# Performance work log

Measured on AMD Instinct MI355X. Metric: run time of the kernel, lower is better.

Reference implementation:

```python
import jax, jax.numpy as jnp
import numpy as np

N_CLASS = 32000
EMB = 1024
HID = 1024
BATCH = 256
SEQ = 256


def setup_inputs() -> dict:
    key = jax.random.key(0)
    ks = jax.random.split(key, 16)
    s = 0.02
    inp = {
        "X": jax.random.randint(ks[0], (BATCH, SEQ), 0, N_CLASS, dtype=jnp.int32),
        "C": jax.random.normal(ks[1], (N_CLASS, EMB), dtype=jnp.float32) * s,
    }
    gate_names = ["W_i1", "W_f1", "W_o1", "W_g1", "W_i2", "W_f2", "W_o2", "W_g2"]
    for i, n in enumerate(gate_names):
        inp[n] = jax.random.normal(ks[2 + i], (HID, EMB + HID), dtype=jnp.float32) * s
    # biases are initialized to ones in the original module
    for n in ["b_i1", "b_f1", "b_o1", "b_g1", "b_i2", "b_f2", "b_o2", "b_g2"]:
        inp[n] = jnp.ones((HID,), dtype=jnp.float32)
    inp["W_out"] = jax.random.normal(ks[10], (N_CLASS, HID), dtype=jnp.float32) * s
    inp["b_out"] = jnp.ones((N_CLASS,), dtype=jnp.float32)
    return inp


def _lstm_dir(Xt, Wi, bi, Wf, bf, Wo, bo, Wg, bg):
    """Run one LSTM direction over Xt: [T, B, E]. Returns final hidden [B, H]."""
    B = Xt.shape[1]
    H = bi.shape[0]
    h0 = jnp.zeros((B, H), Xt.dtype)
    c0 = jnp.zeros((B, H), Xt.dtype)

    def step(carry, x):
        h, c = carry
        xh = jnp.concatenate([x, h], axis=1)  # [B, E+H]
        i = jax.nn.sigmoid(xh @ Wi.T + bi)
        f = jax.nn.sigmoid(xh @ Wf.T + bf)
        o = jax.nn.sigmoid(xh @ Wo.T + bo)
        g = jnp.tanh(xh @ Wg.T + bg)
        c_new = f * c + i * g
        h_new = o * jnp.tanh(c_new)
        return (h_new, c_new), None

    (h, c), _ = jax.lax.scan(step, (h0, c0), Xt)
    return h


def reference(X, C, W_i1, W_f1, W_o1, W_g1, W_i2, W_f2, W_o2, W_g2,
              b_i1, b_f1, b_o1, b_g1, b_i2, b_f2, b_o2, b_g2, W_out, b_out):
    E = C[X]                       # [B, S, E] embedding lookup
    Xt = jnp.transpose(E, (1, 0, 2))  # [T, B, E]
    # forward direction
    h1 = _lstm_dir(Xt, W_i1, b_i1, W_f1, b_f1, W_o1, b_o1, W_g1, b_g1)
    # backward direction: original code detaches (numpy round-trip) before reversing
    Xr = jax.lax.stop_gradient(Xt)[::-1]
    h2 = _lstm_dir(Xr, W_i2, b_i2, W_f2, b_f2, W_o2, b_o2, W_g2, b_g2)
    return (h1 + h2) @ W_out.T + b_out  # [B, n_class]
```

## Files before the change

kernel.cpp:

```cpp
#include <hip/hip_runtime.h>
#include <hip/hip_bf16.h>
#include <stdint.h>
#include <math.h>

#define BATCH 256
#define SEQ   256
#define EMB   1024
#define HID   1024
#define NCLASS 32000
#define KTOT  2048
#define NGATE 8192

typedef __attribute__((ext_vector_type(8))) short bf16x8;
typedef __attribute__((ext_vector_type(4))) float f32x4;

__device__ __forceinline__ unsigned short f2b(float f) {
  union { float f; unsigned u; } v; v.f = f;
  unsigned r = v.u + 0x7FFFu + ((v.u >> 16) & 1u);
  return (unsigned short)(r >> 16);
}
__device__ __forceinline__ float b2f(unsigned short s) {
  union { unsigned u; float f; } v; v.u = ((unsigned)s) << 16;
  return v.f;
}
__device__ __forceinline__ void load_lds16(const void* g, void* l) {
  __builtin_amdgcn_global_load_lds(
      (const __attribute__((address_space(1))) unsigned int*)g,
      (__attribute__((address_space(3))) unsigned int*)l, 16, 0, 0);
}

__global__ void embed_kernel(const int* __restrict__ X, const float* __restrict__ C,
                             unsigned short* __restrict__ Xt) {
  int n = blockIdx.x;
  int t = n >> 8, b = n & 255;
  int tok = X[(size_t)b * SEQ + t];
  float4 v = ((const float4*)(C + (size_t)tok * EMB))[threadIdx.x];
  ushort4 o;
  o.x = f2b(v.x); o.y = f2b(v.y); o.z = f2b(v.z); o.w = f2b(v.w);
  ((ushort4*)(Xt + (size_t)n * EMB))[threadIdx.x] = o;
}

__global__ void castf_kernel(const float* __restrict__ src, unsigned short* __restrict__ dst,
                             int n4) {
  int i = blockIdx.x * blockDim.x + threadIdx.x;
  if (i < n4) {
    float4 v = ((const float4*)src)[i];
    ushort4 o;
    o.x = f2b(v.x); o.y = f2b(v.y); o.z = f2b(v.z); o.w = f2b(v.w);
    ((ushort4*)dst)[i] = o;
  }
}

__global__ void bcat_kernel(const float* b0, const float* b1, const float* b2,
                            const float* b3, const float* b4, const float* b5,
                            const float* b6, const float* b7, float* __restrict__ bcat) {
  int n = blockIdx.x * 256 + threadIdx.x;
  const float* bp[8] = {b0, b1, b2, b3, b4, b5, b6, b7};
  bcat[n] = bp[n >> 10][n & 1023];
}

__launch_bounds__(256)
__global__ void gx_gemm_kernel(const unsigned short* __restrict__ A,
                               const unsigned short* __restrict__ Bw,
                               const float* __restrict__ bcat,
                               unsigned short* __restrict__ Gx) {
  __shared__ unsigned short As[2][128][64];
  __shared__ unsigned short Bs[2][128][64];
  int bid = blockIdx.x;
  int m0 = (bid >> 6) * 128;
  int n0 = (bid & 63) * 128;
  int tid = threadIdx.x;

  auto stage = [&](int buf, int kb) {
    int kbase = kb * 64;
#pragma unroll
    for (int ri = 0; ri < 4; ++ri) {
      int slot = ri * 256 + tid;
      int row = slot >> 3;
      int ce  = (slot & 7) * 8;
      load_lds16(A + (size_t)(m0 + row) * EMB + kbase + ce, &As[buf][row][ce]);
    }
#pragma unroll
    for (int ri = 0; ri < 4; ++ri) {
      int slot = ri * 256 + tid;
      int row = slot >> 3;
      int ce  = (slot & 7) * 8;
      load_lds16(Bw + (size_t)(n0 + row) * KTOT + kbase + ce, &Bs[buf][row][ce]);
    }
  };

  int w = tid >> 6, lane = tid & 63;
  int lm = lane & 15, lq = lane >> 4;
  int wm = w & 1, wn = w >> 1;

  f32x4 zero = {0.f, 0.f, 0.f, 0.f};
  f32x4 acc[4][4];
#pragma unroll
  for (int mi = 0; mi < 4; ++mi)
#pragma unroll
    for (int ni = 0; ni < 4; ++ni) acc[mi][ni] = zero;

  stage(0, 0);
  for (int kb = 0; kb < 16; ++kb) {
    int cur = kb & 1;
    __syncthreads();
    if (kb + 1 < 16) stage(1 - cur, kb + 1);
#pragma unroll
    for (int kc = 0; kc < 2; ++kc) {
      bf16x8 af[4];
#pragma unroll
      for (int mi = 0; mi < 4; ++mi)
        af[mi] = *(const bf16x8*)&As[cur][wm * 64 + mi * 16 + lm][kc * 32 + lq * 8];
#pragma unroll
      for (int ni = 0; ni < 4; ++ni) {
        bf16x8 bb = *(const bf16x8*)&Bs[cur][wn * 64 + ni * 16 + lm][kc * 32 + lq * 8];
#pragma unroll
        for (int mi = 0; mi < 4; ++mi)
          acc[mi][ni] = __builtin_amdgcn_mfma_f32_16x16x32_bf16(af[mi], bb, acc[mi][ni], 0, 0, 0);
      }
    }
  }

#pragma unroll
  for (int ni = 0; ni < 4; ++ni) {
    int n = n0 + wn * 64 + ni * 16 + lm;
    float bn = bcat[n];
#pragma unroll
    for (int mi = 0; mi < 4; ++mi) {
#pragma unroll
      for (int reg = 0; reg < 4; ++reg) {
        int m = m0 + wm * 64 + mi * 16 + lq * 4 + reg;
        Gx[(size_t)m * NGATE + n] = f2b(acc[mi][ni][reg] + bn);
      }
    }
  }
}

#define BM 128
#define BN 64
#define BK 64
__launch_bounds__(256)
__global__ void lstm_step_kernel(const unsigned short* __restrict__ Xt,
                                 const unsigned short* __restrict__ Wcat,
                                 const unsigned short* __restrict__ Gx,
                                 const unsigned short* __restrict__ h_in,
                                 unsigned short* __restrict__ h_out,
                                 float* __restrict__ c_st,
                                 const float* __restrict__ b0, const float* __restrict__ b1,
                                 const float* __restrict__ b2, const float* __restrict__ b3,
                                 const float* __restrict__ b4, const float* __restrict__ b5,
                                 const float* __restrict__ b6, const float* __restrict__ b7,
                                 int t) {
  __shared__ unsigned short As[2][BM][BK];
  __shared__ unsigned short Bs[2][BN][BK];

  int bid = blockIdx.x;
  int d   = bid >> 7;
  int r   = bid & 127;
  int m0  = (r & 1) * BM;
  int j0  = (r >> 1) * 16;
  int td  = d ? (SEQ - 1 - t) : t;
  int tid = threadIdx.x;

  bool useGx = (Gx != nullptr);
  int  kiters = useGx ? (HID / BK) : (KTOT / BK);
  int  koff   = useGx ? EMB : 0;

  const unsigned short* Asrc0 = Xt  + ((size_t)td * BATCH + m0) * EMB;
  const unsigned short* Asrc1 = h_in + ((size_t)d * BATCH + m0) * HID;
  const unsigned short* Wd    = Wcat + (size_t)d * 4 * HID * KTOT;

  auto stageA = [&](int buf, int kb) {
    int kbase = kb * BK;
    const unsigned short* src; int ko;
    if (useGx)            { src = Asrc1; ko = kbase; }
    else if (kbase < EMB) { src = Asrc0; ko = kbase; }
    else                  { src = Asrc1; ko = kbase - EMB; }
#pragma unroll
    for (int ri = 0; ri < 4; ++ri) {
      int slot = ri * 256 + tid;
      int row = slot >> 3;
      int ce  = (slot & 7) * 8;
      load_lds16(src + (size_t)row * 1024 + ko + ce, &As[buf][row][ce]);
    }
  };
  auto stageB = [&](int buf, int kb) {
    int kbase = koff + kb * BK;
#pragma unroll
    for (int ri = 0; ri < 2; ++ri) {
      int slot = ri * 256 + tid;
      int rr  = slot >> 3;
      int g8  = rr >> 4;
      int jj  = rr & 15;
      int ce  = (slot & 7) * 8;
      load_lds16(Wd + (size_t)(g8 * HID + j0 + jj) * KTOT + kbase + ce, &Bs[buf][rr][ce]);
    }
  };

  int w = tid >> 6, lane = tid & 63;
  int lm = lane & 15, lq = lane >> 4;

  f32x4 zero = {0.f, 0.f, 0.f, 0.f};
  f32x4 acc[2][4];
#pragma unroll
  for (int mi = 0; mi < 2; ++mi)
#pragma unroll
    for (int g8 = 0; g8 < 4; ++g8) acc[mi][g8] = zero;

  stageA(0, 0); stageB(0, 0);
  for (int kb = 0; kb < kiters; ++kb) {
    int cur = kb & 1;
    __syncthreads();
    if (kb + 1 < kiters) { stageA(1 - cur, kb + 1); stageB(1 - cur, kb + 1); }
#pragma unroll
    for (int kc = 0; kc < 2; ++kc) {
      bf16x8 a0 = *(const bf16x8*)&As[cur][w * 32 +  0 + lm][kc * 32 + lq * 8];
      bf16x8 a1 = *(const bf16x8*)&As[cur][w * 32 + 16 + lm][kc * 32 + lq * 8];
#pragma unroll
      for (int g8 = 0; g8 < 4; ++g8) {
        bf16x8 bb = *(const bf16x8*)&Bs[cur][g8 * 16 + lm][kc * 32 + lq * 8];
        acc[0][g8] = __builtin_amdgcn_mfma_f32_16x16x32_bf16(a0, bb, acc[0][g8], 0, 0, 0);
        acc[1][g8] = __builtin_amdgcn_mfma_f32_16x16x32_bf16(a1, bb, acc[1][g8], 0, 0, 0);
      }
    }
  }

  const float* bi = d ? b4 : b0;
  const float* bf = d ? b5 : b1;
  const float* bo = d ? b6 : b2;
  const float* bgp= d ? b7 : b3;
  int j = j0 + lm;
  float vbi, vbf, vbo, vbg;
  if (!useGx) { vbi = bi[j]; vbf = bf[j]; vbo = bo[j]; vbg = bgp[j]; }
  else        { vbi = vbf = vbo = vbg = 0.f; }
  const unsigned short* gxb = nullptr;
  if (useGx)
    gxb = Gx + (size_t)td * BATCH * NGATE + (size_t)d * 4096 + j0 + lm;

#pragma unroll
  for (int mi = 0; mi < 2; ++mi) {
#pragma unroll
    for (int reg = 0; reg < 4; ++reg) {
      int b = m0 + w * 32 + mi * 16 + lq * 4 + reg;
      float pi = acc[mi][0][reg] + vbi;
      float pf = acc[mi][1][reg] + vbf;
      float po = acc[mi][2][reg] + vbo;
      float pg = acc[mi][3][reg] + vbg;
      if (useGx) {
        const unsigned short* g = gxb + (size_t)b * NGATE;
        pi += b2f(g[0]);
        pf += b2f(g[1024]);
        po += b2f(g[2048]);
        pg += b2f(g[3072]);
      }
      float ig = 1.f / (1.f + __expf(-pi));
      float fg = 1.f / (1.f + __expf(-pf));
      float og = 1.f / (1.f + __expf(-po));
      float gg = tanhf(pg);
      size_t ci = ((size_t)d * BATCH + b) * HID + j;
      float cn = fg * c_st[ci] + ig * gg;
      c_st[ci] = cn;
      h_out[ci] = f2b(og * tanhf(cn));
    }
  }
}

__global__ void hsum_kernel(const unsigned short* __restrict__ hfin,
                            unsigned short* __restrict__ hs) {
  int i = blockIdx.x * 256 + threadIdx.x;
  ushort4 a = ((const ushort4*)hfin)[i];
  ushort4 b = ((const ushort4*)(hfin + (size_t)BATCH * HID))[i];
  ushort4 o;
  o.x = f2b(b2f(a.x) + b2f(b.x));
  o.y = f2b(b2f(a.y) + b2f(b.y));
  o.z = f2b(b2f(a.z) + b2f(b.z));
  o.w = f2b(b2f(a.w) + b2f(b.w));
  ((ushort4*)hs)[i] = o;
}

__launch_bounds__(256)
__global__ void out_gemm_kernel(const unsigned short* __restrict__ A,
                                const unsigned short* __restrict__ B,
                                const float* __restrict__ bias,
                                float* __restrict__ Cout) {
  __shared__ unsigned short As[2][128][64];
  __shared__ unsigned short Bs[2][128][64];
  int bid = blockIdx.x;
  int m0 = (bid & 1) * 128;
  int n0 = (bid >> 1) * 128;
  int tid = threadIdx.x;

  auto stage = [&](int buf, int kb) {
    int kbase = kb * 64;
#pragma unroll
    for (int ri = 0; ri < 4; ++ri) {
      int slot = ri * 256 + tid;
      int row = slot >> 3;
      int ce  = (slot & 7) * 8;
      load_lds16(A + ((size_t)(m0 + row)) * HID + kbase + ce, &As[buf][row][ce]);
    }
#pragma unroll
    for (int ri = 0; ri < 4; ++ri) {
      int slot = ri * 256 + tid;
      int row = slot >> 3;
      int ce  = (slot & 7) * 8;
      load_lds16(B + ((size_t)(n0 + row)) * HID + kbase + ce, &Bs[buf][row][ce]);
    }
  };

  int w = tid >> 6, lane = tid & 63;
  int lm = lane & 15, lq = lane >> 4;
  int wm = w & 1, wn = w >> 1;

  f32x4 zero = {0.f, 0.f, 0.f, 0.f};
  f32x4 acc[4][4];
#pragma unroll
  for (int mi = 0; mi < 4; ++mi)
#pragma unroll
    for (int ni = 0; ni < 4; ++ni) acc[mi][ni] = zero;

  stage(0, 0);
  for (int kb = 0; kb < 16; ++kb) {
    int cur = kb & 1;
    __syncthreads();
    if (kb + 1 < 16) stage(1 - cur, kb + 1);
#pragma unroll
    for (int kc = 0; kc < 2; ++kc) {
      bf16x8 af[4];
#pragma unroll
      for (int mi = 0; mi < 4; ++mi)
        af[mi] = *(const bf16x8*)&As[cur][wm * 64 + mi * 16 + lm][kc * 32 + lq * 8];
#pragma unroll
      for (int ni = 0; ni < 4; ++ni) {
        bf16x8 bb = *(const bf16x8*)&Bs[cur][wn * 64 + ni * 16 + lm][kc * 32 + lq * 8];
#pragma unroll
        for (int mi = 0; mi < 4; ++mi)
          acc[mi][ni] = __builtin_amdgcn_mfma_f32_16x16x32_bf16(af[mi], bb, acc[mi][ni], 0, 0, 0);
      }
    }
  }

#pragma unroll
  for (int ni = 0; ni < 4; ++ni) {
    int n = n0 + wn * 64 + ni * 16 + lm;
    float bn = bias[n];
#pragma unroll
    for (int mi = 0; mi < 4; ++mi) {
#pragma unroll
      for (int reg = 0; reg < 4; ++reg) {
        int m = m0 + wm * 64 + mi * 16 + lq * 4 + reg;
        Cout[(size_t)m * NCLASS + n] = acc[mi][ni][reg] + bn;
      }
    }
  }
}

extern "C" void kernel_launch(void* const* d_in, const int* in_sizes, int n_in,
                              void* d_out, int out_size, void* d_ws, size_t ws_size,
                              hipStream_t stream) {
  const int*   X    = (const int*)d_in[0];
  const float* C    = (const float*)d_in[1];
  const float* Wg[8];
  for (int i = 0; i < 8; ++i) Wg[i] = (const float*)d_in[2 + i];
  const float* bg[8];
  for (int i = 0; i < 8; ++i) bg[i] = (const float*)d_in[10 + i];
  const float* Wout = (const float*)d_in[18];
  const float* bout = (const float*)d_in[19];
  float* out = (float*)d_out;

  const size_t szXt   = (size_t)SEQ * BATCH * EMB * 2;
  const size_t szWcat = (size_t)8 * HID * KTOT * 2;
  const size_t szWob  = (size_t)NCLASS * HID * 2;
  const size_t szH    = (size_t)2 * BATCH * HID * 2;
  const size_t szC    = (size_t)2 * BATCH * HID * 4;
  const size_t szHs   = (size_t)BATCH * HID * 2;
  const size_t szBc   = (size_t)NGATE * 4;
  const size_t szGx   = (size_t)SEQ * BATCH * NGATE * 2;

  uint8_t* p = (uint8_t*)d_ws;
  unsigned short* Xt   = (unsigned short*)p; p += szXt;
  unsigned short* Wcat = (unsigned short*)p; p += szWcat;
  unsigned short* Wob  = (unsigned short*)p; p += szWob;
  unsigned short* hb0  = (unsigned short*)p; p += szH;
  unsigned short* hb1  = (unsigned short*)p; p += szH;
  float*          cst  = (float*)p;          p += szC;
  unsigned short* hs   = (unsigned short*)p; p += szHs;
  float*          bcat = (float*)p;          p += szBc;
  unsigned short* Gx   = (unsigned short*)p; p += szGx;

  size_t need_full = (size_t)(p - (uint8_t*)d_ws);
  bool useGx = (ws_size >= need_full);
  if (!useGx) Gx = nullptr;

  hipMemsetAsync(hb0, 0, szH, stream);
  hipMemsetAsync(cst, 0, szC, stream);

  embed_kernel<<<SEQ * BATCH, 256, 0, stream>>>(X, C, Xt);
  for (int i = 0; i < 8; ++i)
    castf_kernel<<<2048, 256, 0, stream>>>(Wg[i], Wcat + (size_t)i * HID * KTOT,
                                           (HID * KTOT) / 4);
  castf_kernel<<<32000, 256, 0, stream>>>(Wout, Wob, (NCLASS * HID) / 4);

  if (useGx) {
    bcat_kernel<<<NGATE / 256, 256, 0, stream>>>(bg[0], bg[1], bg[2], bg[3],
                                                 bg[4], bg[5], bg[6], bg[7], bcat);
    gx_gemm_kernel<<<512 * 64, 256, 0, stream>>>(Xt, Wcat, bcat, Gx);
  }

  unsigned short* hbuf[2] = {hb0, hb1};
  for (int t = 0; t < SEQ; ++t) {
    lstm_step_kernel<<<256, 256, 0, stream>>>(
        Xt, Wcat, Gx, hbuf[t & 1], hbuf[(t + 1) & 1], cst,
        bg[0], bg[1], bg[2], bg[3], bg[4], bg[5], bg[6], bg[7], t);
  }
  hsum_kernel<<<256, 256, 0, stream>>>(hb0, hs);
  out_gemm_kernel<<<500, 256, 0, stream>>>(hs, Wob, bout, out);
}
```

Before: 10.52 ms.

## Replace per-step LSTM launches with persistent kernel holding recurrent weights in LDS

Replaces the 256 per-timestep kernel launches with a single persistent kernel of 256 blocks. Each block keeps its slice of the recurrent weights resident in LDS (128KB) and keeps the cell state in registers. Blocks synchronise between timesteps with a per-group global atomic barrier. The input-projection GEMM output is re-laid out so each block reads its gate values contiguously. This removes launch overhead and the repeated reloading of recurrent weights from global memory. In exchange it relies on all blocks being co-resident, and it uses fast tanh approximations.

```diff
diff --git a/kernel.cpp b/kernel.cpp
--- a/kernel.cpp
+++ b/kernel.cpp
@@ -27,6 +27,9 @@
   __builtin_amdgcn_global_load_lds(
       (const __attribute__((address_space(1))) unsigned int*)g,
       (__attribute__((address_space(3))) unsigned int*)l, 16, 0, 0);
+}
+__device__ __forceinline__ float tanh_fast(float x) {
+  return 1.f - 2.f / (__expf(2.f * x) + 1.f);
 }
 
 __global__ void embed_kernel(const int* __restrict__ X, const float* __restrict__ C,
@@ -63,7 +66,7 @@
 __global__ void gx_gemm_kernel(const unsigned short* __restrict__ A,
                                const unsigned short* __restrict__ Bw,
                                const float* __restrict__ bcat,
-                               unsigned short* __restrict__ Gx) {
+                               unsigned short* __restrict__ Gx2) {
   __shared__ unsigned short As[2][128][64];
   __shared__ unsigned short Bs[2][128][64];
   int bid = blockIdx.x;
@@ -121,18 +124,171 @@
     }
   }
 
+  int tt  = m0 >> 8;
+  int mhb = m0 & 255;
 #pragma unroll
   for (int ni = 0; ni < 4; ++ni) {
-    int n = n0 + wn * 64 + ni * 16 + lm;
+    int n  = n0 + wn * 64 + ni * 16 + lm;
     float bn = bcat[n];
+    int nb  = n0 + wn * 64 + ni * 16;
+    int d   = nb >> 12;
+    int g   = (nb >> 10) & 3;
+    int ugx = (nb >> 4) & 63;
+    unsigned short* gdst = Gx2 +
+        (((size_t)(tt * 2 + d) * 64 + ugx) * 256) * 64 + g * 16 + lm;
 #pragma unroll
     for (int mi = 0; mi < 4; ++mi) {
 #pragma unroll
       for (int reg = 0; reg < 4; ++reg) {
-        int m = m0 + wm * 64 + mi * 16 + lq * 4 + reg;
-        Gx[(size_t)m * NGATE + n] = f2b(acc[mi][ni][reg] + bn);
-      }
-    }
+        int bloc = mhb + wm * 64 + mi * 16 + lq * 4 + reg;
+        gdst[(size_t)bloc * 64] = f2b(acc[mi][ni][reg] + bn);
+      }
+    }
+  }
+}
+
+__launch_bounds__(256, 1)
+__global__ void lstm_persist(const unsigned short* __restrict__ Wcat,
+                             const unsigned short* __restrict__ Gx2,
+                             unsigned short* __restrict__ hb0,
+                             unsigned short* __restrict__ hb1,
+                             unsigned int* __restrict__ bar) {
+  __shared__ unsigned short Wlds[64 * 1024];
+  __shared__ unsigned short As[2][4096];
+
+  const int bid = blockIdx.x;
+  const int dir = bid >> 7;
+  const int mh  = (bid >> 6) & 1;
+  const int ug  = bid & 63;
+  const int j0  = ug * 16;
+  const int grp = bid >> 6;
+  const int tid = threadIdx.x;
+  const int w   = tid >> 6;
+  const int lane = tid & 63;
+  const int lm = lane & 15, lq = lane >> 4;
+
+  const unsigned short* Wd = Wcat + (size_t)dir * 4 * HID * KTOT;
+
+#pragma unroll
+  for (int i = 0; i < 32; ++i) {
+    int s = i * 256 + tid;
+    int P = s << 4;
+    int n = P >> 11;
+    int offl = (P & 2047) ^ ((n & 7) << 4);
+    int g = n >> 4, u = n & 15;
+    load_lds16(Wd + (size_t)(g * HID + j0 + u) * KTOT + EMB + (offl >> 1),
+               Wlds + (P >> 1));
+  }
+
+  int sp0 = 0, sp1 = 0, lp0 = 0, lp1 = 0;
+#pragma unroll
+  for (int r = 0; r < 2; ++r) {
+    int s = r * 256 + tid;
+    int P = s << 4;
+    int r2 = (P >> 8) & 1;
+    int r1 = (P >> 7) & 1;
+    int r0 = ((P >> 6) & 1) ^ r2;
+    int L  = P ^ ((r0 | (r1 << 1) | (r2 << 2)) << 4);
+    int row  = L >> 6;
+    int colb = L & 63;
+    if (r == 0) { sp0 = row * HID + (colb >> 1); lp0 = P >> 1; }
+    else        { sp1 = row * HID + (colb >> 1); lp1 = P >> 1; }
+  }
+
+  int row0 = w * 32 + lm;
+  int row1 = row0 + 16;
+  int aP0 = ((row0 * 64 + lq * 16) ^ ((row0 & 7) << 4)) >> 1;
+  int aP1 = ((row1 * 64 + lq * 16) ^ ((row1 & 7) << 4)) >> 1;
+  int swzB = (lm & 7) << 4;
+
+  float cs[2][4];
+#pragma unroll
+  for (int mi = 0; mi < 2; ++mi)
+#pragma unroll
+    for (int reg = 0; reg < 4; ++reg) cs[mi][reg] = 0.f;
+
+  const int rbb = w * 32 + lq * 4;
+  const size_t hblk = ((size_t)dir * 256 + mh * 128) * 1024;
+  unsigned int tgt = 0;
+  unsigned int* barp = bar + grp * 32;
+
+  __syncthreads();
+
+  for (int t = 0; t < SEQ; ++t) {
+    int td = dir ? (SEQ - 1 - t) : t;
+    const unsigned short* hprev = ((t & 1) ? hb1 : hb0) + hblk;
+    unsigned short*       hnext = ((t & 1) ? hb0 : hb1) + hblk;
+
+    const unsigned short* gxt = Gx2 +
+        ((((size_t)td * 2 + dir) * 64 + ug) * 256 + mh * 128) * 64 + lm;
+    unsigned short gxr[2][4][4];
+#pragma unroll
+    for (int mi = 0; mi < 2; ++mi)
+#pragma unroll
+      for (int reg = 0; reg < 4; ++reg) {
+        const unsigned short* gp = gxt + (size_t)(rbb + mi * 16 + reg) * 64;
+#pragma unroll
+        for (int g = 0; g < 4; ++g) gxr[mi][g][reg] = gp[g * 16];
+      }
+
+    f32x4 acc[2][4];
+#pragma unroll
+    for (int mi = 0; mi < 2; ++mi)
+#pragma unroll
+      for (int g = 0; g < 4; ++g) acc[mi][g] = (f32x4){0.f, 0.f, 0.f, 0.f};
+
+    if (t) {
+      load_lds16(hprev + sp0, &As[0][0] + lp0);
+      load_lds16(hprev + sp1, &As[0][0] + lp1);
+      for (int kb = 0; kb < 32; ++kb) {
+        int cur = kb & 1;
+        __syncthreads();
+        if (kb + 1 < 32) {
+          const unsigned short* hsrc = hprev + (kb + 1) * 32;
+          load_lds16(hsrc + sp0, &As[1 - cur][0] + lp0);
+          load_lds16(hsrc + sp1, &As[1 - cur][0] + lp1);
+        }
+        bf16x8 a0 = *(const bf16x8*)&As[cur][aP0];
+        bf16x8 a1 = *(const bf16x8*)&As[cur][aP1];
+        int off = ((kb * 64 + lq * 16) ^ swzB) >> 1;
+#pragma unroll
+        for (int g = 0; g < 4; ++g) {
+          bf16x8 bb = *(const bf16x8*)&Wlds[(g * 16 + lm) * 1024 + off];
+          acc[0][g] = __builtin_amdgcn_mfma_f32_16x16x32_bf16(a0, bb, acc[0][g], 0, 0, 0);
+          acc[1][g] = __builtin_amdgcn_mfma_f32_16x16x32_bf16(a1, bb, acc[1][g], 0, 0, 0);
+        }
+      }
+    }
+
+#pragma unroll
+    for (int mi = 0; mi < 2; ++mi) {
+#pragma unroll
+      for (int reg = 0; reg < 4; ++reg) {
+        float pi = acc[mi][0][reg] + b2f(gxr[mi][0][reg]);
+        float pf = acc[mi][1][reg] + b2f(gxr[mi][1][reg]);
+        float po = acc[mi][2][reg] + b2f(gxr[mi][2][reg]);
+        float pg = acc[mi][3][reg] + b2f(gxr[mi][3][reg]);
+        float ig = 1.f / (1.f + __expf(-pi));
+        float fg = 1.f / (1.f + __expf(-pf));
+        float og = 1.f / (1.f + __expf(-po));
+        float gg = tanh_fast(pg);
+        float cn = fg * cs[mi][reg] + ig * gg;
+        cs[mi][reg] = cn;
+        int rb = rbb + mi * 16 + reg;
+        hnext[(size_t)rb * 1024 + j0 + lm] = f2b(og * tanh_fast(cn));
+      }
+    }
+
+    tgt += 64;
+    __syncthreads();
+    if (tid == 0) {
+      __threadfence();
+      atomicAdd(barp, 1u);
+      while (__hip_atomic_load(barp, __ATOMIC_RELAXED,
+                               __HIP_MEMORY_SCOPE_AGENT) < tgt) {}
+    }
+    __syncthreads();
+    __threadfence();
   }
 }
 
@@ -233,9 +389,6 @@
   float vbi, vbf, vbo, vbg;
   if (!useGx) { vbi = bi[j]; vbf = bf[j]; vbo = bo[j]; vbg = bgp[j]; }
   else        { vbi = vbf = vbo = vbg = 0.f; }
-  const unsigned short* gxb = nullptr;
-  if (useGx)
-    gxb = Gx + (size_t)td * BATCH * NGATE + (size_t)d * 4096 + j0 + lm;
 
 #pragma unroll
   for (int mi = 0; mi < 2; ++mi) {
@@ -246,13 +399,6 @@
       float pf = acc[mi][1][reg] + vbf;
       float po = acc[mi][2][reg] + vbo;
       float pg = acc[mi][3][reg] + vbg;
-      if (useGx) {
-        const unsigned short* g = gxb + (size_t)b * NGATE;
-        pi += b2f(g[0]);
-        pf += b2f(g[1024]);
-        po += b2f(g[2048]);
-        pg += b2f(g[3072]);
-      }
       float ig = 1.f / (1.f + __expf(-pi));
       float fg = 1.f / (1.f + __expf(-pf));
       float og = 1.f / (1.f + __expf(-po));
@@ -405,13 +551,15 @@
     bcat_kernel<<<NGATE / 256, 256, 0, stream>>>(bg[0], bg[1], bg[2], bg[3],
                                                  bg[4], bg[5], bg[6], bg[7], bcat);
     gx_gemm_kernel<<<512 * 64, 256, 0, stream>>>(Xt, Wcat, bcat, Gx);
-  }
-
-  unsigned short* hbuf[2] = {hb0, hb1};
-  for (int t = 0; t < SEQ; ++t) {
-    lstm_step_kernel<<<256, 256, 0, stream>>>(
-        Xt, Wcat, Gx, hbuf[t & 1], hbuf[(t + 1) & 1], cst,
-        bg[0], bg[1], bg[2], bg[3], bg[4], bg[5], bg[6], bg[7], t);
+    unsigned int* bar = (unsigned int*)cst;
+    lstm_persist<<<256, 256, 0, stream>>>(Wcat, Gx, hb0, hb1, bar);
+  } else {
+    unsigned short* hbuf[2] = {hb0, hb1};
+    for (int t = 0; t < SEQ; ++t) {
+      lstm_step_kernel<<<256, 256, 0, stream>>>(
+          Xt, Wcat, Gx, hbuf[t & 1], hbuf[(t + 1) & 1], cst,
+          bg[0], bg[1], bg[2], bg[3], bg[4], bg[5], bg[6], bg[7], t);
+    }
   }
   hsum_kernel<<<256, 256, 0, stream>>>(hb0, hs);
   out_gemm_kernel<<<500, 256, 0, stream>>>(hs, Wob, bout, out);
```

After: 10.41 ms. About the same (-1.1%).

## Replace per-step LSTM launches with persistent kernel holding Wh in LDS

Applied to the files above, without the earlier changes.

Replaces the precomputed Gx GEMM and the 256 per-timestep launches with one persistent kernel of 256 blocks. Each block keeps its slice of the recurrent weights resident in a swizzled 128KB LDS buffer and holds the cell state in registers. The next step's input projection is computed while waiting on per-group atomic flags, so it overlaps the cross-block sync. This removes the large Gx round trip through memory and the launch overhead. The risks are that all blocks must be co-resident for the spin barrier, the spin loop has a bounded iteration count, and tanh now uses a fast exp-based approximation.

```diff
diff --git a/kernel.cpp b/kernel.cpp
--- a/kernel.cpp
+++ b/kernel.cpp
@@ -9,7 +9,6 @@
 #define HID   1024
 #define NCLASS 32000
 #define KTOT  2048
-#define NGATE 8192
 
 typedef __attribute__((ext_vector_type(8))) short bf16x8;
 typedef __attribute__((ext_vector_type(4))) float f32x4;
@@ -27,6 +26,9 @@
   __builtin_amdgcn_global_load_lds(
       (const __attribute__((address_space(1))) unsigned int*)g,
       (__attribute__((address_space(3))) unsigned int*)l, 16, 0, 0);
+}
+__device__ __forceinline__ float tanh_fast(float x) {
+  return 1.f - 2.f / (__expf(2.f * x) + 1.f);
 }
 
 __global__ void embed_kernel(const int* __restrict__ X, const float* __restrict__ C,
@@ -51,216 +53,181 @@
   }
 }
 
-__global__ void bcat_kernel(const float* b0, const float* b1, const float* b2,
-                            const float* b3, const float* b4, const float* b5,
-                            const float* b6, const float* b7, float* __restrict__ bcat) {
-  int n = blockIdx.x * 256 + threadIdx.x;
-  const float* bp[8] = {b0, b1, b2, b3, b4, b5, b6, b7};
-  bcat[n] = bp[n >> 10][n & 1023];
-}
-
-__launch_bounds__(256)
-__global__ void gx_gemm_kernel(const unsigned short* __restrict__ A,
-                               const unsigned short* __restrict__ Bw,
-                               const float* __restrict__ bcat,
-                               unsigned short* __restrict__ Gx) {
-  __shared__ unsigned short As[2][128][64];
-  __shared__ unsigned short Bs[2][128][64];
-  int bid = blockIdx.x;
-  int m0 = (bid >> 6) * 128;
-  int n0 = (bid & 63) * 128;
-  int tid = threadIdx.x;
-
-  auto stage = [&](int buf, int kb) {
-    int kbase = kb * 64;
-#pragma unroll
-    for (int ri = 0; ri < 4; ++ri) {
-      int slot = ri * 256 + tid;
-      int row = slot >> 3;
-      int ce  = (slot & 7) * 8;
-      load_lds16(A + (size_t)(m0 + row) * EMB + kbase + ce, &As[buf][row][ce]);
-    }
-#pragma unroll
-    for (int ri = 0; ri < 4; ++ri) {
-      int slot = ri * 256 + tid;
-      int row = slot >> 3;
-      int ce  = (slot & 7) * 8;
-      load_lds16(Bw + (size_t)(n0 + row) * KTOT + kbase + ce, &Bs[buf][row][ce]);
+__launch_bounds__(256, 1)
+__global__ void lstm_persist2(const unsigned short* __restrict__ Xt,
+                              const unsigned short* __restrict__ Wcat,
+                              const float* __restrict__ b0, const float* __restrict__ b1,
+                              const float* __restrict__ b2, const float* __restrict__ b3,
+                              const float* __restrict__ b4, const float* __restrict__ b5,
+                              const float* __restrict__ b6, const float* __restrict__ b7,
+                              unsigned short* __restrict__ hb0,
+                              unsigned short* __restrict__ hb1,
+                              unsigned int* __restrict__ flags) {
+  __shared__ unsigned short Whlds[64 * 1024];
+  __shared__ unsigned short Bxs[2][4096];
+
+  const int bid = blockIdx.x;
+  const int dir = bid >> 7;
+  const int mh  = (bid >> 6) & 1;
+  const int ug  = bid & 63;
+  const int j0  = ug * 16;
+  const int tid = threadIdx.x;
+  const int w   = tid >> 6;
+  const int lane = tid & 63;
+  const int lm = lane & 15, lq = lane >> 4;
+
+  const unsigned short* Wd = Wcat + (size_t)dir * 4 * HID * KTOT;
+
+#pragma unroll
+  for (int i = 0; i < 32; ++i) {
+    int P = (i * 256 + tid) << 4;
+    int row = P >> 11;
+    int offl = (P & 2047) ^ ((row & 7) << 4);
+    int g = row >> 4, u = row & 15;
+    load_lds16(Wd + (size_t)(g * HID + j0 + u) * KTOT + EMB + (offl >> 1),
+               &Whlds[P >> 1]);
+  }
+
+  const unsigned short* bxsrc[2];
+  int bxdst[2];
+#pragma unroll
+  for (int r = 0; r < 2; ++r) {
+    int P = (r * 256 + tid) << 4;
+    int row = P >> 7;
+    int L = P ^ ((row & 7) << 4);
+    int g = row >> 4, u = row & 15;
+    bxsrc[r] = Wd + (size_t)(g * HID + j0 + u) * KTOT + ((L & 127) >> 1);
+    bxdst[r] = P >> 1;
+  }
+
+  const int swz = (lm & 7) << 4;
+  const int r0off = (w * 32 + lm) * 1024 + lq * 8;
+  const int r1off = r0off + 16 * 1024;
+
+  const float* pbi = dir ? b4 : b0;
+  const float* pbf = dir ? b5 : b1;
+  const float* pbo = dir ? b6 : b2;
+  const float* pbg = dir ? b7 : b3;
+  const float vbi = pbi[j0 + lm], vbf = pbf[j0 + lm];
+  const float vbo = pbo[j0 + lm], vbg = pbg[j0 + lm];
+
+  f32x4 acc[2][4];
+  float cs[2][4];
+#pragma unroll
+  for (int mi = 0; mi < 2; ++mi)
+#pragma unroll
+    for (int reg = 0; reg < 4; ++reg) cs[mi][reg] = 0.f;
+
+  const size_t hblk = ((size_t)dir * BATCH + mh * 128) * HID;
+  unsigned int* fgrp = flags + (bid & ~63);
+  const int rbb = w * 32 + lq * 4;
+
+  auto xphase = [&](int td) {
+    const unsigned short* xs = Xt + ((size_t)td * BATCH + mh * 128) * EMB;
+#pragma unroll
+    for (int mi = 0; mi < 2; ++mi)
+#pragma unroll
+      for (int g = 0; g < 4; ++g) acc[mi][g] = (f32x4){0.f, 0.f, 0.f, 0.f};
+    load_lds16(bxsrc[0], &Bxs[0][bxdst[0]]);
+    load_lds16(bxsrc[1], &Bxs[0][bxdst[1]]);
+    bf16x8 xc00 = *(const bf16x8*)(xs + r0off);
+    bf16x8 xc01 = *(const bf16x8*)(xs + r1off);
+    bf16x8 xc10 = *(const bf16x8*)(xs + r0off + 32);
+    bf16x8 xc11 = *(const bf16x8*)(xs + r1off + 32);
+#pragma unroll
+    for (int ch = 0; ch < 16; ++ch) {
+      int cur = ch & 1;
+      __syncthreads();
+      bf16x8 xn00 = xc00, xn01 = xc01, xn10 = xc10, xn11 = xc11;
+      if (ch < 15) {
+        load_lds16(bxsrc[0] + (ch + 1) * 64, &Bxs[1 - cur][bxdst[0]]);
+        load_lds16(bxsrc[1] + (ch + 1) * 64, &Bxs[1 - cur][bxdst[1]]);
+        int ko = (ch + 1) * 64;
+        xn00 = *(const bf16x8*)(xs + r0off + ko);
+        xn01 = *(const bf16x8*)(xs + r1off + ko);
+        xn10 = *(const bf16x8*)(xs + r0off + ko + 32);
+        xn11 = *(const bf16x8*)(xs + r1off + ko + 32);
+      }
+#pragma unroll
+      for (int kc = 0; kc < 2; ++kc) {
+        bf16x8 a0 = kc ? xc10 : xc00;
+        bf16x8 a1 = kc ? xc11 : xc01;
+#pragma unroll
+        for (int g = 0; g < 4; ++g) {
+          int offB = (((g * 16 + lm) * 128 + kc * 64 + lq * 16) ^ swz) >> 1;
+          bf16x8 bb = *(const bf16x8*)&Bxs[cur][offB];
+          acc[0][g] = __builtin_amdgcn_mfma_f32_16x16x32_bf16(a0, bb, acc[0][g], 0, 0, 0);
+          acc[1][g] = __builtin_amdgcn_mfma_f32_16x16x32_bf16(a1, bb, acc[1][g], 0, 0, 0);
+        }
+      }
+      xc00 = xn00; xc01 = xn01; xc10 = xn10; xc11 = xn11;
     }
   };
 
-  int w = tid >> 6, lane = tid & 63;
-  int lm = lane & 15, lq = lane >> 4;
-  int wm = w & 1, wn = w >> 1;
-
-  f32x4 zero = {0.f, 0.f, 0.f, 0.f};
-  f32x4 acc[4][4];
-#pragma unroll
-  for (int mi = 0; mi < 4; ++mi)
-#pragma unroll
-    for (int ni = 0; ni < 4; ++ni) acc[mi][ni] = zero;
-
-  stage(0, 0);
-  for (int kb = 0; kb < 16; ++kb) {
-    int cur = kb & 1;
-    __syncthreads();
-    if (kb + 1 < 16) stage(1 - cur, kb + 1);
-#pragma unroll
-    for (int kc = 0; kc < 2; ++kc) {
-      bf16x8 af[4];
-#pragma unroll
-      for (int mi = 0; mi < 4; ++mi)
-        af[mi] = *(const bf16x8*)&As[cur][wm * 64 + mi * 16 + lm][kc * 32 + lq * 8];
-#pragma unroll
-      for (int ni = 0; ni < 4; ++ni) {
-        bf16x8 bb = *(const bf16x8*)&Bs[cur][wn * 64 + ni * 16 + lm][kc * 32 + lq * 8];
-#pragma unroll
-        for (int mi = 0; mi < 4; ++mi)
-          acc[mi][ni] = __builtin_amdgcn_mfma_f32_16x16x32_bf16(af[mi], bb, acc[mi][ni], 0, 0, 0);
-      }
-    }
-  }
-
-#pragma unroll
-  for (int ni = 0; ni < 4; ++ni) {
-    int n = n0 + wn * 64 + ni * 16 + lm;
-    float bn = bcat[n];
-#pragma unroll
-    for (int mi = 0; mi < 4; ++mi) {
+  auto hphase = [&](const unsigned short* hp) {
+    bf16x8 ac0 = *(const bf16x8*)(hp + r0off);
+    bf16x8 ac1 = *(const bf16x8*)(hp + r1off);
+#pragma unroll
+    for (int kb = 0; kb < 32; ++kb) {
+      bf16x8 an0 = ac0, an1 = ac1;
+      if (kb < 31) {
+        an0 = *(const bf16x8*)(hp + r0off + (kb + 1) * 32);
+        an1 = *(const bf16x8*)(hp + r1off + (kb + 1) * 32);
+      }
+      int offW = ((kb * 64 + lq * 16) ^ swz) >> 1;
+#pragma unroll
+      for (int g = 0; g < 4; ++g) {
+        bf16x8 bb = *(const bf16x8*)&Whlds[(g * 16 + lm) * 1024 + offW];
+        acc[0][g] = __builtin_amdgcn_mfma_f32_16x16x32_bf16(ac0, bb, acc[0][g], 0, 0, 0);
+        acc[1][g] = __builtin_amdgcn_mfma_f32_16x16x32_bf16(ac1, bb, acc[1][g], 0, 0, 0);
+      }
+      ac0 = an0; ac1 = an1;
+    }
+  };
+
+  xphase(dir ? SEQ - 1 : 0);
+
+  for (int t = 0; t < SEQ; ++t) {
+    if (t > 0) hphase(((t & 1) ? hb1 : hb0) + hblk);
+    unsigned short* hnext = ((t & 1) ? hb0 : hb1) + hblk;
+
+#pragma unroll
+    for (int mi = 0; mi < 2; ++mi) {
 #pragma unroll
       for (int reg = 0; reg < 4; ++reg) {
-        int m = m0 + wm * 64 + mi * 16 + lq * 4 + reg;
-        Gx[(size_t)m * NGATE + n] = f2b(acc[mi][ni][reg] + bn);
-      }
-    }
-  }
-}
-
-#define BM 128
-#define BN 64
-#define BK 64
-__launch_bounds__(256)
-__global__ void lstm_step_kernel(const unsigned short* __restrict__ Xt,
-                                 const unsigned short* __restrict__ Wcat,
-                                 const unsigned short* __restrict__ Gx,
-                                 const unsigned short* __restrict__ h_in,
-                                 unsigned short* __restrict__ h_out,
-                                 float* __restrict__ c_st,
-                                 const float* __restrict__ b0, const float* __restrict__ b1,
-                                 const float* __restrict__ b2, const float* __restrict__ b3,
-                                 const float* __restrict__ b4, const float* __restrict__ b5,
-                                 const float* __restrict__ b6, const float* __restrict__ b7,
-                                 int t) {
-  __shared__ unsigned short As[2][BM][BK];
-  __shared__ unsigned short Bs[2][BN][BK];
-
-  int bid = blockIdx.x;
-  int d   = bid >> 7;
-  int r   = bid & 127;
-  int m0  = (r & 1) * BM;
-  int j0  = (r >> 1) * 16;
-  int td  = d ? (SEQ - 1 - t) : t;
-  int tid = threadIdx.x;
-
-  bool useGx = (Gx != nullptr);
-  int  kiters = useGx ? (HID / BK) : (KTOT / BK);
-  int  koff   = useGx ? EMB : 0;
-
-  const unsigned short* Asrc0 = Xt  + ((size_t)td * BATCH + m0) * EMB;
-  const unsigned short* Asrc1 = h_in + ((size_t)d * BATCH + m0) * HID;
-  const unsigned short* Wd    = Wcat + (size_t)d * 4 * HID * KTOT;
-
-  auto stageA = [&](int buf, int kb) {
-    int kbase = kb * BK;
-    const unsigned short* src; int ko;
-    if (useGx)            { src = Asrc1; ko = kbase; }
-    else if (kbase < EMB) { src = Asrc0; ko = kbase; }
-    else                  { src = Asrc1; ko = kbase - EMB; }
-#pragma unroll
-    for (int ri = 0; ri < 4; ++ri) {
-      int slot = ri * 256 + tid;
-      int row = slot >> 3;
-      int ce  = (slot & 7) * 8;
-      load_lds16(src + (size_t)row * 1024 + ko + ce, &As[buf][row][ce]);
-    }
-  };
-  auto stageB = [&](int buf, int kb) {
-    int kbase = koff + kb * BK;
-#pragma unroll
-    for (int ri = 0; ri < 2; ++ri) {
-      int slot = ri * 256 + tid;
-      int rr  = slot >> 3;
-      int g8  = rr >> 4;
-      int jj  = rr & 15;
-      int ce  = (slot & 7) * 8;
-      load_lds16(Wd + (size_t)(g8 * HID + j0 + jj) * KTOT + kbase + ce, &Bs[buf][rr][ce]);
-    }
-  };
-
-  int w = tid >> 6, lane = tid & 63;
-  int lm = lane & 15, lq = lane >> 4;
-
-  f32x4 zero = {0.f, 0.f, 0.f, 0.f};
-  f32x4 acc[2][4];
-#pragma unroll
-  for (int mi = 0; mi < 2; ++mi)
-#pragma unroll
-    for (int g8 = 0; g8 < 4; ++g8) acc[mi][g8] = zero;
-
-  stageA(0, 0); stageB(0, 0);
-  for (int kb = 0; kb < kiters; ++kb) {
-    int cur = kb & 1;
-    __syncthreads();
-    if (kb + 1 < kiters) { stageA(1 - cur, kb + 1); stageB(1 - cur, kb + 1); }
-#pragma unroll
-    for (int kc = 0; kc < 2; ++kc) {
-      bf16x8 a0 = *(const bf16x8*)&As[cur][w * 32 +  0 + lm][kc * 32 + lq * 8];
-      bf16x8 a1 = *(const bf16x8*)&As[cur][w * 32 + 16 + lm][kc * 32 + lq * 8];
-#pragma unroll
-      for (int g8 = 0; g8 < 4; ++g8) {
-        bf16x8 bb = *(const bf16x8*)&Bs[cur][g8 * 16 + lm][kc * 32 + lq * 8];
-        acc[0][g8] = __builtin_amdgcn_mfma_f32_16x16x32_bf16(a0, bb, acc[0][g8], 0, 0, 0);
-        acc[1][g8] = __builtin_amdgcn_mfma_f32_16x16x32_bf16(a1, bb, acc[1][g8], 0, 0, 0);
-      }
-    }
-  }
-
-  const float* bi = d ? b4 : b0;
-  const float* bf = d ? b5 : b1;
-  const float* bo = d ? b6 : b2;
-  const float* bgp= d ? b7 : b3;
-  int j = j0 + lm;
-  float vbi, vbf, vbo, vbg;
-  if (!useGx) { vbi = bi[j]; vbf = bf[j]; vbo = bo[j]; vbg = bgp[j]; }
-  else        { vbi = vbf = vbo = vbg = 0.f; }
-  const unsigned short* gxb = nullptr;
-  if (useGx)
-    gxb = Gx + (size_t)td * BATCH * NGATE + (size_t)d * 4096 + j0 + lm;
-
-#pragma unroll
-  for (int mi = 0; mi < 2; ++mi) {
-#pragma unroll
-    for (int reg = 0; reg < 4; ++reg) {
-      int b = m0 + w * 32 + mi * 16 + lq * 4 + reg;
-      float pi = acc[mi][0][reg] + vbi;
-      float pf = acc[mi][1][reg] + vbf;
-      float po = acc[mi][2][reg] + vbo;
-      float pg = acc[mi][3][reg] + vbg;
-      if (useGx) {
-        const unsigned short* g = gxb + (size_t)b * NGATE;
-        pi += b2f(g[0]);
-        pf += b2f(g[1024]);
-        po += b2f(g[2048]);
-        pg += b2f(g[3072]);
-      }
-      float ig = 1.f / (1.f + __expf(-pi));
-      float fg = 1.f / (1.f + __expf(-pf));
-      float og = 1.f / (1.f + __expf(-po));
-      float gg = tanhf(pg);
-      size_t ci = ((size_t)d * BATCH + b) * HID + j;
-      float cn = fg * c_st[ci] + ig * gg;
-      c_st[ci] = cn;
-      h_out[ci] = f2b(og * tanhf(cn));
+        float pi = acc[mi][0][reg] + vbi;
+        float pf = acc[mi][1][reg] + vbf;
+        float po = acc[mi][2][reg] + vbo;
+        float pg = acc[mi][3][reg] + vbg;
+        float ig = 1.f / (1.f + __expf(-pi));
+        float fg = 1.f / (1.f + __expf(-pf));
+        float og = 1.f / (1.f + __expf(-po));
+        float gg = tanh_fast(pg);
+        float cn = fg * cs[mi][reg] + ig * gg;
+        cs[mi][reg] = cn;
+        int rb = rbb + mi * 16 + reg;
+        hnext[(size_t)rb * HID + j0 + lm] = f2b(og * tanh_fast(cn));
+      }
+    }
+
+    if (t < SEQ - 1) {
+      __syncthreads();
+      if (tid == 0) {
+        __threadfence();
+        __hip_atomic_store(&flags[bid], (unsigned)(t + 1),
+                           __ATOMIC_RELEASE, __HIP_MEMORY_SCOPE_AGENT);
+      }
+      xphase(dir ? (SEQ - 2 - t) : (t + 1));
+      if (tid < 64) {
+        unsigned tgt = (unsigned)(t + 1);
+        for (int spin = 0; spin < (1 << 16); ++spin) {
+          unsigned v = __hip_atomic_load(&fgrp[tid], __ATOMIC_ACQUIRE,
+                                         __HIP_MEMORY_SCOPE_AGENT);
+          if (__all((int)(v >= tgt))) break;
+        }
+      }
+      __syncthreads();
+      __threadfence();
     }
   }
 }
@@ -372,10 +339,8 @@
   const size_t szWcat = (size_t)8 * HID * KTOT * 2;
   const size_t szWob  = (size_t)NCLASS * HID * 2;
   const size_t szH    = (size_t)2 * BATCH * HID * 2;
-  const size_t szC    = (size_t)2 * BATCH * HID * 4;
+  const size_t szFl   = 4096;
   const size_t szHs   = (size_t)BATCH * HID * 2;
-  const size_t szBc   = (size_t)NGATE * 4;
-  const size_t szGx   = (size_t)SEQ * BATCH * NGATE * 2;
 
   uint8_t* p = (uint8_t*)d_ws;
   unsigned short* Xt   = (unsigned short*)p; p += szXt;
@@ -383,17 +348,10 @@
   unsigned short* Wob  = (unsigned short*)p; p += szWob;
   unsigned short* hb0  = (unsigned short*)p; p += szH;
   unsigned short* hb1  = (unsigned short*)p; p += szH;
-  float*          cst  = (float*)p;          p += szC;
+  unsigned int*   flags= (unsigned int*)p;   p += szFl;
   unsigned short* hs   = (unsigned short*)p; p += szHs;
-  float*          bcat = (float*)p;          p += szBc;
-  unsigned short* Gx   = (unsigned short*)p; p += szGx;
-
-  size_t need_full = (size_t)(p - (uint8_t*)d_ws);
-  bool useGx = (ws_size >= need_full);
-  if (!useGx) Gx = nullptr;
-
-  hipMemsetAsync(hb0, 0, szH, stream);
-  hipMemsetAsync(cst, 0, szC, stream);
+
+  hipMemsetAsync(flags, 0, szFl, stream);
 
   embed_kernel<<<SEQ * BATCH, 256, 0, stream>>>(X, C, Xt);
   for (int i = 0; i < 8; ++i)
@@ -401,18 +359,11 @@
                                            (HID * KTOT) / 4);
   castf_kernel<<<32000, 256, 0, stream>>>(Wout, Wob, (NCLASS * HID) / 4);
 
-  if (useGx) {
-    bcat_kernel<<<NGATE / 256, 256, 0, stream>>>(bg[0], bg[1], bg[2], bg[3],
-                                                 bg[4], bg[5], bg[6], bg[7], bcat);
-    gx_gemm_kernel<<<512 * 64, 256, 0, stream>>>(Xt, Wcat, bcat, Gx);
-  }
-
-  unsigned short* hbuf[2] = {hb0, hb1};
-  for (int t = 0; t < SEQ; ++t) {
-    lstm_step_kernel<<<256, 256, 0, stream>>>(
-        Xt, Wcat, Gx, hbuf[t & 1], hbuf[(t + 1) & 1], cst,
-        bg[0], bg[1], bg[2], bg[3], bg[4], bg[5], bg[6], bg[7], t);
-  }
+  lstm_persist2<<<256, 256, 0, stream>>>(
+      Xt, Wcat,
+      bg[0], bg[1], bg[2], bg[3], bg[4], bg[5], bg[6], bg[7],
+      hb0, hb1, flags);
+
   hsum_kernel<<<256, 256, 0, stream>>>(hb0, hs);
   out_gemm_kernel<<<500, 256, 0, stream>>>(hs, Wob, bout, out);
 }
```

Result: slower. 14.28 ms (+35.8%).
